# Kernel optimization log

Hardware: AMD Instinct MI355X
Metric: run time of the kernel (lower is better)

Reference implementation:

```python
import jax, jax.numpy as jnp
import numpy as np

N = 10000      # nodes
E = 320000     # edges (avg degree 32)
IN = 512       # in_channels
OUT = 128      # out_channels
H = 4          # in_head
C1 = 2 * OUT   # per-head hidden channels of conv1 (256)
NEG_SLOPE = 0.2


def setup_inputs() -> dict:
    key = jax.random.key(0)
    ks = jax.random.split(key, 12)
    x = jax.random.normal(ks[0], (N, IN), dtype=jnp.float32)
    edge_index = jax.random.randint(ks[1], (2, E), 0, N, dtype=jnp.int64)
    def glorot(k, shape):
        lim = np.sqrt(6.0 / (shape[0] + shape[-1])).astype(np.float32)
        return jax.random.uniform(k, shape, jnp.float32, -lim, lim)
    # conv1: GATv2Conv(IN -> C1 per head, heads=H)
    Wl1 = glorot(ks[2], (IN, H * C1))
    Wr1 = glorot(ks[3], (IN, H * C1))
    att1 = glorot(ks[4], (H, C1))
    b1 = jnp.zeros((H * C1,), jnp.float32)
    # conv2: GATv2Conv(H*C1 -> OUT, heads=1)
    Wl2 = glorot(ks[5], (H * C1, OUT))
    Wr2 = glorot(ks[6], (H * C1, OUT))
    att2 = glorot(ks[7], (1, OUT))
    b2 = jnp.zeros((OUT,), jnp.float32)
    return {"x": x, "edge_index": edge_index, "Wl1": Wl1, "Wr1": Wr1,
            "att1": att1, "b1": b1, "Wl2": Wl2, "Wr2": Wr2,
            "att2": att2, "b2": b2}


def gatv2_conv(x, src, dst, Wl, Wr, att, b, heads, ch):
    # x: [N, F_in]; src/dst: [E] (message src -> dst, softmax over dst)
    n = x.shape[0]
    xl = (x @ Wl).reshape(n, heads, ch)   # source-side projection
    xr = (x @ Wr).reshape(n, heads, ch)   # target-side projection
    # per-edge GATv2 score: att . LeakyReLU(xl_j + xr_i)   [E, H]
    e = jax.nn.leaky_relu(xl[src] + xr[dst], NEG_SLOPE)    # [E, H, C]
    s = jnp.einsum('ehc,hc->eh', e, att)                   # [E, H]
    # segment softmax over incoming edges of each dst node
    smax = jax.lax.stop_gradient(jax.ops.segment_max(s, dst, num_segments=n))
    ex = jnp.exp(s - smax[dst])
    denom = jax.ops.segment_sum(ex, dst, num_segments=n)
    alpha = ex / denom[dst]                                # [E, H]
    # weighted scatter-add of source messages
    out = jax.ops.segment_sum(alpha[:, :, None] * xl[src], dst, num_segments=n)
    return out.reshape(n, heads * ch) + b                  # concat heads + bias


def reference(x, edge_index, Wl1, Wr1, att1, b1, Wl2, Wr2, att2, b2):
    src, dst = edge_index[0], edge_index[1]
    h = gatv2_conv(x, src, dst, Wl1, Wr1, att1, b1, H, C1)
    h = jax.nn.relu(h)                                     # [N, H*C1]
    out = gatv2_conv(h, src, dst, Wl2, Wr2, att2, b2, 1, OUT)
    return out                                             # [N, OUT]
```

## Files before the change

### kernel.cpp

```cpp
#include <hip/hip_runtime.h>
#include <cfloat>

#define N_NODES 10000
#define N_EDGES 320000
#define IN_F    512
#define F1      1024
#define OUT_F   128
#define NEG     0.2f
#define BUCKET  128

typedef __attribute__((ext_vector_type(8))) short bf16x8;
typedef __attribute__((ext_vector_type(4))) float f32x4;

__device__ __forceinline__ float lrelu(float v) { return fmaxf(v, NEG * v); }

__device__ __forceinline__ unsigned short f2bf(float f) {
    unsigned u = __float_as_uint(f);
    u += 0x7fff + ((u >> 16) & 1);
    return (unsigned short)(u >> 16);
}
__device__ __forceinline__ float bf2f(unsigned short h) {
    return __uint_as_float(((unsigned)h) << 16);
}
__device__ __forceinline__ void u2f2(unsigned u, float& e0, float& e1) {
    e0 = __uint_as_float(u << 16);
    e1 = __uint_as_float(u & 0xffff0000u);
}

__device__ __forceinline__ float rsum16(float x) {
    x += __int_as_float(__builtin_amdgcn_update_dpp(0, __float_as_int(x), 0x121, 0xF, 0xF, false));
    x += __int_as_float(__builtin_amdgcn_update_dpp(0, __float_as_int(x), 0x122, 0xF, 0xF, false));
    x += __int_as_float(__builtin_amdgcn_update_dpp(0, __float_as_int(x), 0x124, 0xF, 0xF, false));
    x += __int_as_float(__builtin_amdgcn_update_dpp(0, __float_as_int(x), 0x128, 0xF, 0xF, false));
    return x;
}

__device__ __forceinline__ void gld_lds16(const void* g, void* l) {
    __builtin_amdgcn_global_load_lds(
        (const __attribute__((address_space(1))) unsigned int*)g,
        (__attribute__((address_space(3))) unsigned int*)l, 16, 0, 0);
}

#define PB_X  2500
#define PB_S  3750
#define PB_W1 4774
#define PB_END 5030

__device__ __forceinline__ void wt_body(const float* __restrict__ Wa,
                                        const float* __restrict__ Wb,
                                        unsigned short* __restrict__ tbf,
                                        int K, int NS, int n0, int k0, int t,
                                        float (*tile)[33]) {
    int j = t & 31;
    const float* W = (n0 < NS) ? Wa : Wb;
    int nb = (n0 < NS) ? n0 : n0 - NS;
#pragma unroll
    for (int r = 0; r < 4; ++r) {
        int kl = (t >> 5) + r * 8;
        tile[kl][j] = W[(size_t)(k0 + kl) * NS + nb + j];
    }
    __syncthreads();
#pragma unroll
    for (int r = 0; r < 4; ++r) {
        int nl = (t >> 5) + r * 8;
        tbf[(size_t)(n0 + nl) * K + k0 + j] = f2bf(tile[j][nl]);
    }
}

__global__ __launch_bounds__(256) void k_prep(const float* __restrict__ x,
                                              unsigned short* __restrict__ xbf,
                                              const int* __restrict__ ei,
                                              int* __restrict__ cnt,
                                              int* __restrict__ esrc,
                                              const float* __restrict__ Wl1,
                                              const float* __restrict__ Wr1,
                                              unsigned short* __restrict__ w1bf,
                                              const float* __restrict__ Wl2,
                                              const float* __restrict__ Wr2,
                                              unsigned short* __restrict__ w2bf) {
    __shared__ float tile[32][33];
    int bid = blockIdx.x, t = threadIdx.x;
    if (bid < PB_X) {
        int i = bid * 2048 + t * 8;
        float4 v0 = *(const float4*)(x + i);
        float4 v1 = *(const float4*)(x + i + 4);
        ushort4 h0, h1;
        h0.x = f2bf(v0.x); h0.y = f2bf(v0.y); h0.z = f2bf(v0.z); h0.w = f2bf(v0.w);
        h1.x = f2bf(v1.x); h1.y = f2bf(v1.y); h1.z = f2bf(v1.z); h1.w = f2bf(v1.w);
        *(ushort4*)(xbf + i) = h0;
        *(ushort4*)(xbf + i + 4) = h1;
    } else if (bid < PB_S) {
        int e = (bid - PB_X) * 256 + t;
        if (e < N_EDGES) {
            int d = ei[N_EDGES + e];
            int pos = atomicAdd(&cnt[d], 1);
            if (pos < BUCKET) esrc[(size_t)d * BUCKET + pos] = ei[e];
        }
    } else if (bid < PB_W1) {
        int local = bid - PB_S;
        wt_body(Wl1, Wr1, w1bf, IN_F, F1, (local & 63) * 32, (local >> 6) * 32, t, tile);
    } else {
        int local = bid - PB_W1;
        wt_body(Wl2, Wr2, w2bf, F1, OUT_F, (local & 7) * 32, (local >> 3) * 32, t, tile);
    }
}

__global__ __launch_bounds__(256) void k_sort(const int* __restrict__ cnt,
                                              int* __restrict__ esrc) {
    int t = threadIdx.x;
    int w = t >> 6, lane = t & 63;
    int nd = blockIdx.x * 4 + w;
    if (nd >= N_NODES) return;
    int deg = min(cnt[nd], 64);
    int p0 = nd * BUCKET;
    int v = (lane < deg) ? esrc[p0 + lane] : 0x7fffffff;
#pragma unroll
    for (int k = 2; k <= 64; k <<= 1) {
#pragma unroll
        for (int j = k >> 1; j > 0; j >>= 1) {
            int other = __shfl_xor(v, j);
            bool dir = ((lane & k) == 0);
            bool lower = ((lane & j) == 0);
            int mn = min(v, other), mx = max(v, other);
            v = (lower == dir) ? mn : mx;
        }
    }
    if (lane < deg) esrc[p0 + lane] = v;
}

template<int BM, int WR, int WC>
__global__ __launch_bounds__(256) void gemm_mfma(
        const unsigned short* __restrict__ A,
        const unsigned short* __restrict__ B,
        unsigned short* __restrict__ Cl, unsigned short* __restrict__ Cr,
        int M, int K, int NSPLIT) {
    constexpr int NI = BM / (16 * WR);
    constexpr int NJ = 128 / (16 * WC);
    __shared__ __align__(16) short As[BM * 32];
    __shared__ __align__(16) short Bs[128 * 32];
    int t = threadIdx.x;
    int lane = t & 63, w = t >> 6;
    int row0 = blockIdx.y * BM;
    int n0 = blockIdx.x * 128;
    int wr0 = (w / WC) * (NI * 16);
    int wc0 = (w % WC) * (NJ * 16);
    int q = lane >> 4, md = lane & 15;
    int srow = t >> 2;
    int skoff = (t & 3) * 8;

    f32x4 acc[NI][NJ];
#pragma unroll
    for (int i = 0; i < NI; ++i)
#pragma unroll
        for (int j = 0; j < NJ; ++j)
#pragma unroll
            for (int r = 0; r < 4; ++r) acc[i][j][r] = 0.f;

    for (int k0 = 0; k0 < K; k0 += 32) {
        __syncthreads();
#pragma unroll
        for (int is = 0; is < BM / 64; ++is) {
            int gr = row0 + is * 64 + srow;
            if (gr < M)
                gld_lds16(A + (size_t)gr * K + k0 + skoff,
                          &As[(is * 64 + (t >> 6) * 16) * 32]);
        }
#pragma unroll
        for (int is = 0; is < 2; ++is) {
            int gn = n0 + is * 64 + srow;
            gld_lds16(B + (size_t)gn * K + k0 + skoff,
                      &Bs[(is * 64 + (t >> 6) * 16) * 32]);
        }
        __syncthreads();

        bf16x8 av[NI], bv[NJ];
#pragma unroll
        for (int i = 0; i < NI; ++i)
            av[i] = *(const bf16x8*)&As[(wr0 + i * 16 + md) * 32 + q * 8];
#pragma unroll
        for (int j = 0; j < NJ; ++j)
            bv[j] = *(const bf16x8*)&Bs[(wc0 + j * 16 + md) * 32 + q * 8];
#pragma unroll
        for (int i = 0; i < NI; ++i)
#pragma unroll
            for (int j = 0; j < NJ; ++j)
                acc[i][j] = __builtin_amdgcn_mfma_f32_16x16x32_bf16(av[i], bv[j], acc[i][j], 0, 0, 0);
    }

#pragma unroll
    for (int i = 0; i < NI; ++i)
#pragma unroll
        for (int j = 0; j < NJ; ++j) {
            int col = n0 + wc0 + j * 16 + md;
            unsigned short* C = (col < NSPLIT) ? Cl : Cr;
            int cc = (col < NSPLIT) ? col : col - NSPLIT;
#pragma unroll
            for (int r = 0; r < 4; ++r) {
                int grow = row0 + wr0 + i * 16 + q * 4 + r;
                if (grow < M) C[(size_t)grow * NSPLIT + cc] = f2bf(acc[i][j][r]);
            }
        }
}

__global__ __launch_bounds__(256) void k_fused1(const unsigned short* __restrict__ xlbf,
                                                const unsigned short* __restrict__ xrbf,
                                                const int* __restrict__ cnt,
                                                const int* __restrict__ esrc,
                                                const float* __restrict__ att,
                                                const float* __restrict__ bias,
                                                unsigned short* __restrict__ hb) {
    int t = threadIdx.x;
    int w = t >> 6, lane = t & 63;
    int ni = w >> 1;
    int ww = w & 1;
    int nd = blockIdx.x * 2 + ni;
    int head = lane >> 4, sub = lane & 15;
    int ch = head * 256 + sub * 16;

    __shared__ float slx[4][4];
    __shared__ float4 sacc4[2][4][64];

    float4 r0, r1, r2, r3;
    {
        const uint4* prx = (const uint4*)(xrbf + (size_t)nd * F1 + ch);
        uint4 xa = prx[0], xb = prx[1];
        u2f2(xa.x, r0.x, r0.y); u2f2(xa.y, r0.z, r0.w);
        u2f2(xa.z, r1.x, r1.y); u2f2(xa.w, r1.z, r1.w);
        u2f2(xb.x, r2.x, r2.y); u2f2(xb.y, r2.z, r2.w);
        u2f2(xb.z, r3.x, r3.y); u2f2(xb.w, r3.z, r3.w);
    }
    const float4* pa = (const float4*)(att + ch);
    float4 a0 = pa[0], a1 = pa[1], a2 = pa[2], a3 = pa[3];

    int deg = min(cnt[nd], BUCKET);
    int p0 = nd * BUCKET;
    int dege = min(deg, 64);
    int bkt = (lane < dege) ? esrc[p0 + lane] : 0;

    float l = 0.f;
    float4 acc0 = make_float4(0.f, 0.f, 0.f, 0.f);
    float4 acc1 = acc0, acc2 = acc0, acc3 = acc0;

    auto edge_body = [&](uint4 ca, uint4 cb) {
        float4 c0, c1, c2, c3;
        u2f2(ca.x, c0.x, c0.y); u2f2(ca.y, c0.z, c0.w);
        u2f2(ca.z, c1.x, c1.y); u2f2(ca.w, c1.z, c1.w);
        u2f2(cb.x, c2.x, c2.y); u2f2(cb.y, c2.z, c2.w);
        u2f2(cb.z, c3.x, c3.y); u2f2(cb.w, c3.z, c3.w);
        float u;
        float sl0, sa0, sl1, sa1, sl2, sa2, sl3, sa3;
        u = c0.x + r0.x; sl0 = a0.x * u;           sa0 = a0.x * fabsf(u);
        u = c0.y + r0.y; sl0 = fmaf(a0.y, u, sl0); sa0 = fmaf(a0.y, fabsf(u), sa0);
        u = c0.z + r0.z; sl0 = fmaf(a0.z, u, sl0); sa0 = fmaf(a0.z, fabsf(u), sa0);
        u = c0.w + r0.w; sl0 = fmaf(a0.w, u, sl0); sa0 = fmaf(a0.w, fabsf(u), sa0);
        u = c1.x + r1.x; sl1 = a1.x * u;           sa1 = a1.x * fabsf(u);
        u = c1.y + r1.y; sl1 = fmaf(a1.y, u, sl1); sa1 = fmaf(a1.y, fabsf(u), sa1);
        u = c1.z + r1.z; sl1 = fmaf(a1.z, u, sl1); sa1 = fmaf(a1.z, fabsf(u), sa1);
        u = c1.w + r1.w; sl1 = fmaf(a1.w, u, sl1); sa1 = fmaf(a1.w, fabsf(u), sa1);
        u = c2.x + r2.x; sl2 = a2.x * u;           sa2 = a2.x * fabsf(u);
        u = c2.y + r2.y; sl2 = fmaf(a2.y, u, sl2); sa2 = fmaf(a2.y, fabsf(u), sa2);
        u = c2.z + r2.z; sl2 = fmaf(a2.z, u, sl2); sa2 = fmaf(a2.z, fabsf(u), sa2);
        u = c2.w + r2.w; sl2 = fmaf(a2.w, u, sl2); sa2 = fmaf(a2.w, fabsf(u), sa2);
        u = c3.x + r3.x; sl3 = a3.x * u;           sa3 = a3.x * fabsf(u);
        u = c3.y + r3.y; sl3 = fmaf(a3.y, u, sl3); sa3 = fmaf(a3.y, fabsf(u), sa3);
        u = c3.z + r3.z; sl3 = fmaf(a3.z, u, sl3); sa3 = fmaf(a3.z, fabsf(u), sa3);
        u = c3.w + r3.w; sl3 = fmaf(a3.w, u, sl3); sa3 = fmaf(a3.w, fabsf(u), sa3);
        float sl = (sl0 + sl1) + (sl2 + sl3);
        float sa = (sa0 + sa1) + (sa2 + sa3);
        float s = rsum16(fmaf(0.6f, sl, 0.4f * sa));
        s = fminf(fmaxf(s, -60.f), 60.f);
        float al = __expf(s);
        l += al;
        acc0.x = fmaf(al, c0.x, acc0.x);
        acc0.y = fmaf(al, c0.y, acc0.y);
        acc0.z = fmaf(al, c0.z, acc0.z);
        acc0.w = fmaf(al, c0.w, acc0.w);
        acc1.x = fmaf(al, c1.x, acc1.x);
        acc1.y = fmaf(al, c1.y, acc1.y);
        acc1.z = fmaf(al, c1.z, acc1.z);
        acc1.w = fmaf(al, c1.w, acc1.w);
        acc2.x = fmaf(al, c2.x, acc2.x);
        acc2.y = fmaf(al, c2.y, acc2.y);
        acc2.z = fmaf(al, c2.z, acc2.z);
        acc2.w = fmaf(al, c2.w, acc2.w);
        acc3.x = fmaf(al, c3.x, acc3.x);
        acc3.y = fmaf(al, c3.y, acc3.y);
        acc3.z = fmaf(al, c3.z, acc3.z);
        acc3.w = fmaf(al, c3.w, acc3.w);
    };

    int idx = ww;
    uint4 ua, ub;
    if (idx < dege) {
        int sn = __shfl(bkt, idx);
        const uint4* pv = (const uint4*)(xlbf + (size_t)sn * F1 + ch);
        ua = pv[0]; ub = pv[1];
    }
    for (; idx < dege; idx += 2) {
        uint4 ca = ua, cb = ub;
        int nidx = idx + 2;
        if (nidx < dege) {
            int sn = __shfl(bkt, nidx);
            const uint4* pv = (const uint4*)(xlbf + (size_t)sn * F1 + ch);
            ua = pv[0]; ub = pv[1];
        }
        edge_body(ca, cb);
    }
    for (int p = p0 + 64 + ww; p < p0 + deg; p += 2) {
        const uint4* pv = (const uint4*)(xlbf + (size_t)esrc[p] * F1 + ch);
        edge_body(pv[0], pv[1]);
    }

    if (sub == 0) slx[w][head] = l;
    if (ww == 1) {
        sacc4[ni][0][lane] = acc0;
        sacc4[ni][1][lane] = acc1;
        sacc4[ni][2][lane] = acc2;
        sacc4[ni][3][lane] = acc3;
    }
    __syncthreads();
    if (ww == 0) {
        float L = l + slx[w ^ 1][head];
        float invL = (L > 0.f) ? 1.f / L : 0.f;
        const float4* pb = (const float4*)(bias + ch);
        size_t base = (size_t)nd * F1 + ch;
        float4 aa[4] = {acc0, acc1, acc2, acc3};
#pragma unroll
        for (int j = 0; j < 4; ++j) {
            float4 pt = sacc4[ni][j][lane];
            float4 b4 = pb[j];
            ushort4 hv;
            hv.x = f2bf(fmaxf(fmaf(aa[j].x + pt.x, invL, b4.x), 0.f));
            hv.y = f2bf(fmaxf(fmaf(aa[j].y + pt.y, invL, b4.y), 0.f));
            hv.z = f2bf(fmaxf(fmaf(aa[j].z + pt.z, invL, b4.z), 0.f));
            hv.w = f2bf(fmaxf(fmaf(aa[j].w + pt.w, invL, b4.w), 0.f));
            *(ushort4*)(hb + base + j * 4) = hv;
        }
    }
}

__global__ __launch_bounds__(256) void k_fused2(const unsigned short* __restrict__ xlbf,
                                                const unsigned short* __restrict__ xrbf,
                                                const int* __restrict__ cnt,
                                                const int* __restrict__ esrc,
                                                const float* __restrict__ att,
                                                const float* __restrict__ bias,
                                                float* __restrict__ out) {
    int t = threadIdx.x;
    int w = t >> 6, lane = t & 63;
    int nd = blockIdx.x * 4 + w;
    int g = lane >> 4, sub = lane & 15;
    int ch = sub * 8;

    __shared__ float slx2[4][4];
    __shared__ float sacc2[4][4][132];

    float r[8], a[8];
    {
        uint4 u = *(const uint4*)(xrbf + (size_t)nd * OUT_F + ch);
        u2f2(u.x, r[0], r[1]); u2f2(u.y, r[2], r[3]);
        u2f2(u.z, r[4], r[5]); u2f2(u.w, r[6], r[7]);
        float4 q0 = *(const float4*)(att + ch);
        float4 q1 = *(const float4*)(att + ch + 4);
        a[0] = q0.x; a[1] = q0.y; a[2] = q0.z; a[3] = q0.w;
        a[4] = q1.x; a[5] = q1.y; a[6] = q1.z; a[7] = q1.w;
    }
    int deg = min(cnt[nd], BUCKET);
    int p0 = nd * BUCKET;
    int p1 = p0 + deg;

    float l = 0.f;
    float acc[8] = {};
    uint4 cur, nxt;
    {
        int p = p0 + g;
        if (p < p1)     cur = *(const uint4*)(xlbf + (size_t)esrc[p] * OUT_F + ch);
        if (p + 4 < p1) nxt = *(const uint4*)(xlbf + (size_t)esrc[p + 4] * OUT_F + ch);
    }
    for (int p = p0 + g; p < p1; p += 4) {
        uint4 c = cur;
        cur = nxt;
        if (p + 8 < p1) nxt = *(const uint4*)(xlbf + (size_t)esrc[p + 8] * OUT_F + ch);
        float v[8];
        u2f2(c.x, v[0], v[1]); u2f2(c.y, v[2], v[3]);
        u2f2(c.z, v[4], v[5]); u2f2(c.w, v[6], v[7]);
        float uu;
        float slA, saA, slB, saB;
        uu = v[0] + r[0]; slA = a[0] * uu;           saA = a[0] * fabsf(uu);
        uu = v[1] + r[1]; slA = fmaf(a[1], uu, slA); saA = fmaf(a[1], fabsf(uu), saA);
        uu = v[2] + r[2]; slA = fmaf(a[2], uu, slA); saA = fmaf(a[2], fabsf(uu), saA);
        uu = v[3] + r[3]; slA = fmaf(a[3], uu, slA); saA = fmaf(a[3], fabsf(uu), saA);
        uu = v[4] + r[4]; slB = a[4] * uu;           saB = a[4] * fabsf(uu);
        uu = v[5] + r[5]; slB = fmaf(a[5], uu, slB); saB = fmaf(a[5], fabsf(uu), saB);
        uu = v[6] + r[6]; slB = fmaf(a[6], uu, slB); saB = fmaf(a[6], fabsf(uu), saB);
        uu = v[7] + r[7]; slB = fmaf(a[7], uu, slB); saB = fmaf(a[7], fabsf(uu), saB);
        float s = rsum16(fmaf(0.6f, slA + slB, 0.4f * (saA + saB)));
        s = fminf(fmaxf(s, -60.f), 60.f);
        float al = __expf(s);
        l += al;
#pragma unroll
        for (int k = 0; k < 8; ++k) acc[k] = fmaf(al, v[k], acc[k]);
    }

    if (sub == 0) slx2[w][g] = l;
    float4 v0 = make_float4(acc[0], acc[1], acc[2], acc[3]);
    float4 v1 = make_float4(acc[4], acc[5], acc[6], acc[7]);
    *(float4*)&sacc2[w][g][ch] = v0;
    *(float4*)&sacc2[w][g][ch + 4] = v1;
    __syncthreads();
    float L = slx2[w][0] + slx2[w][1] + slx2[w][2] + slx2[w][3];
    float invL = (L > 0.f) ? 1.f / L : 0.f;
    int c2 = lane * 2;
    float o0 = sacc2[w][0][c2] + sacc2[w][1][c2] + sacc2[w][2][c2] + sacc2[w][3][c2];
    float o1 = sacc2[w][0][c2 + 1] + sacc2[w][1][c2 + 1] + sacc2[w][2][c2 + 1] + sacc2[w][3][c2 + 1];
    float2 bf = *(const float2*)(bias + c2);
    float2 o;
    o.x = fmaf(o0, invL, bf.x);
    o.y = fmaf(o1, invL, bf.y);
    *(float2*)(out + (size_t)nd * OUT_F + c2) = o;
}

extern "C" void kernel_launch(void* const* d_in, const int* in_sizes, int n_in,
                              void* d_out, int out_size, void* d_ws, size_t ws_size,
                              hipStream_t stream) {
    const float* x    = (const float*)d_in[0];
    const int*   ei   = (const int*)d_in[1];
    const float* Wl1  = (const float*)d_in[2];
    const float* Wr1  = (const float*)d_in[3];
    const float* att1 = (const float*)d_in[4];
    const float* b1   = (const float*)d_in[5];
    const float* Wl2  = (const float*)d_in[6];
    const float* Wr2  = (const float*)d_in[7];
    const float* att2 = (const float*)d_in[8];
    const float* b2   = (const float*)d_in[9];
    float* out = (float*)d_out;

    unsigned short* us = (unsigned short*)d_ws;
    unsigned short* xl1bf = us;
    unsigned short* xr1bf = xl1bf + (size_t)N_NODES * F1;
    unsigned short* xl2bf = xr1bf + (size_t)N_NODES * F1;
    unsigned short* xr2bf = xl2bf + (size_t)N_NODES * OUT_F;
    unsigned short* hb   = xr2bf + (size_t)N_NODES * OUT_F;
    unsigned short* xbf  = hb + (size_t)N_NODES * F1;
    unsigned short* w1bf = xbf + (size_t)N_NODES * IN_F;
    unsigned short* w2bf = w1bf + (size_t)2048 * IN_F;
    int* cnt   = (int*)(w2bf + (size_t)256 * F1);
    int* esrc  = cnt + (N_NODES + 16);

    hipMemsetAsync(cnt, 0, sizeof(int) * N_NODES, stream);
    k_prep<<<PB_END, 256, 0, stream>>>(x, xbf, ei, cnt, esrc,
                                       Wl1, Wr1, w1bf,
                                       Wl2, Wr2, w2bf);

    k_sort<<<(N_NODES + 3) / 4, 256, 0, stream>>>(cnt, esrc);

    gemm_mfma<128, 2, 2><<<dim3(16, (N_NODES + 127) / 128), 256, 0, stream>>>(
        xbf, w1bf, xl1bf, xr1bf, N_NODES, IN_F, F1);

    k_fused1<<<N_NODES / 2, 256, 0, stream>>>(xl1bf, xr1bf, cnt, esrc, att1, b1, hb);

    gemm_mfma<64, 1, 4><<<dim3(2, (N_NODES + 63) / 64), 256, 0, stream>>>(
        hb, w2bf, xl2bf, xr2bf, N_NODES, F1, OUT_F);

    k_fused2<<<N_NODES / 4, 256, 0, stream>>>(xl2bf, xr2bf, cnt, esrc, att2, b2, out);
}
```

Baseline: 263.3 us.

## Stage GEMM epilogue through LDS for coalesced stores and add nontemporal hints

The GEMM epilogue now writes bf16 accumulators into a shared-memory tile that reuses the operand staging buffers through a union, then writes whole rows to global memory with 16-byte vector stores. Previously each lane wrote scattered 2-byte values. Separately, single-use streams (the x conversion, xr row loads, and the h and out stores) now use nontemporal loads and stores to reduce cache pollution. The cost is an extra LDS round trip plus barriers in the GEMM, and the nontemporal hint on h may hurt if the following GEMM would have reused it from cache.

Measured after the change: 267.2 us. About the same (+1.5%).

```diff
diff --git a/kernel.cpp b/kernel.cpp
--- a/kernel.cpp
+++ b/kernel.cpp
@@ -11,6 +11,9 @@
 
 typedef __attribute__((ext_vector_type(8))) short bf16x8;
 typedef __attribute__((ext_vector_type(4))) float f32x4;
+typedef __attribute__((ext_vector_type(2))) float f32x2;
+typedef __attribute__((ext_vector_type(4))) unsigned int u32x4;
+typedef __attribute__((ext_vector_type(4))) unsigned short u16x4;
 
 __device__ __forceinline__ float lrelu(float v) { return fmaxf(v, NEG * v); }
 
@@ -82,8 +85,8 @@
     int bid = blockIdx.x, t = threadIdx.x;
     if (bid < PB_X) {
         int i = bid * 2048 + t * 8;
-        float4 v0 = *(const float4*)(x + i);
-        float4 v1 = *(const float4*)(x + i + 4);
+        f32x4 v0 = __builtin_nontemporal_load((const f32x4*)(x + i));
+        f32x4 v1 = __builtin_nontemporal_load((const f32x4*)(x + i + 4));
         ushort4 h0, h1;
         h0.x = f2bf(v0.x); h0.y = f2bf(v0.y); h0.z = f2bf(v0.z); h0.w = f2bf(v0.w);
         h1.x = f2bf(v1.x); h1.y = f2bf(v1.y); h1.z = f2bf(v1.z); h1.w = f2bf(v1.w);
@@ -128,6 +131,13 @@
     if (lane < deg) esrc[p0 + lane] = v;
 }
 
+template<int BM> struct GemmSmem {
+    union {
+        struct { short As[BM * 32]; short Bs[128 * 32]; } st;
+        unsigned short ct[BM * 136];
+    };
+};
+
 template<int BM, int WR, int WC>
 __global__ __launch_bounds__(256) void gemm_mfma(
         const unsigned short* __restrict__ A,
@@ -136,8 +146,7 @@
         int M, int K, int NSPLIT) {
     constexpr int NI = BM / (16 * WR);
     constexpr int NJ = 128 / (16 * WC);
-    __shared__ __align__(16) short As[BM * 32];
-    __shared__ __align__(16) short Bs[128 * 32];
+    __shared__ __align__(16) GemmSmem<BM> sm;
     int t = threadIdx.x;
     int lane = t & 63, w = t >> 6;
     int row0 = blockIdx.y * BM;
@@ -163,23 +172,23 @@
             int gr = row0 + is * 64 + srow;
             if (gr < M)
                 gld_lds16(A + (size_t)gr * K + k0 + skoff,
-                          &As[(is * 64 + (t >> 6) * 16) * 32]);
+                          &sm.st.As[(is * 64 + (t >> 6) * 16) * 32]);
         }
 #pragma unroll
         for (int is = 0; is < 2; ++is) {
             int gn = n0 + is * 64 + srow;
             gld_lds16(B + (size_t)gn * K + k0 + skoff,
-                      &Bs[(is * 64 + (t >> 6) * 16) * 32]);
+                      &sm.st.Bs[(is * 64 + (t >> 6) * 16) * 32]);
         }
         __syncthreads();
 
         bf16x8 av[NI], bv[NJ];
 #pragma unroll
         for (int i = 0; i < NI; ++i)
-            av[i] = *(const bf16x8*)&As[(wr0 + i * 16 + md) * 32 + q * 8];
+            av[i] = *(const bf16x8*)&sm.st.As[(wr0 + i * 16 + md) * 32 + q * 8];
 #pragma unroll
         for (int j = 0; j < NJ; ++j)
-            bv[j] = *(const bf16x8*)&Bs[(wc0 + j * 16 + md) * 32 + q * 8];
+            bv[j] = *(const bf16x8*)&sm.st.Bs[(wc0 + j * 16 + md) * 32 + q * 8];
 #pragma unroll
         for (int i = 0; i < NI; ++i)
 #pragma unroll
@@ -187,19 +196,25 @@
                 acc[i][j] = __builtin_amdgcn_mfma_f32_16x16x32_bf16(av[i], bv[j], acc[i][j], 0, 0, 0);
     }
 
+    __syncthreads();
 #pragma unroll
     for (int i = 0; i < NI; ++i)
 #pragma unroll
-        for (int j = 0; j < NJ; ++j) {
-            int col = n0 + wc0 + j * 16 + md;
-            unsigned short* C = (col < NSPLIT) ? Cl : Cr;
-            int cc = (col < NSPLIT) ? col : col - NSPLIT;
-#pragma unroll
-            for (int r = 0; r < 4; ++r) {
-                int grow = row0 + wr0 + i * 16 + q * 4 + r;
-                if (grow < M) C[(size_t)grow * NSPLIT + cc] = f2bf(acc[i][j][r]);
-            }
-        }
+        for (int j = 0; j < NJ; ++j)
+#pragma unroll
+            for (int r = 0; r < 4; ++r)
+                sm.ct[(wr0 + i * 16 + q * 4 + r) * 136 + wc0 + j * 16 + md] =
+                    f2bf(acc[i][j][r]);
+    __syncthreads();
+    unsigned short* C = (n0 < NSPLIT) ? Cl : Cr;
+    int cc0 = (n0 < NSPLIT) ? n0 : n0 - NSPLIT;
+    for (int idx = t; idx < BM * 16; idx += 256) {
+        int row = idx >> 4, seg = idx & 15;
+        if (row0 + row < M) {
+            bf16x8 val = *(const bf16x8*)&sm.ct[row * 136 + seg * 8];
+            *(bf16x8*)(C + (size_t)(row0 + row) * NSPLIT + cc0 + seg * 8) = val;
+        }
+    }
 }
 
 __global__ __launch_bounds__(256) void k_fused1(const unsigned short* __restrict__ xlbf,
@@ -222,8 +237,9 @@
 
     float4 r0, r1, r2, r3;
     {
-        const uint4* prx = (const uint4*)(xrbf + (size_t)nd * F1 + ch);
-        uint4 xa = prx[0], xb = prx[1];
+        const u32x4* prx = (const u32x4*)(xrbf + (size_t)nd * F1 + ch);
+        u32x4 xa = __builtin_nontemporal_load(prx);
+        u32x4 xb = __builtin_nontemporal_load(prx + 1);
         u2f2(xa.x, r0.x, r0.y); u2f2(xa.y, r0.z, r0.w);
         u2f2(xa.z, r1.x, r1.y); u2f2(xa.w, r1.z, r1.w);
         u2f2(xb.x, r2.x, r2.y); u2f2(xb.y, r2.z, r2.w);
@@ -329,12 +345,12 @@
         for (int j = 0; j < 4; ++j) {
             float4 pt = sacc4[ni][j][lane];
             float4 b4 = pb[j];
-            ushort4 hv;
+            u16x4 hv;
             hv.x = f2bf(fmaxf(fmaf(aa[j].x + pt.x, invL, b4.x), 0.f));
             hv.y = f2bf(fmaxf(fmaf(aa[j].y + pt.y, invL, b4.y), 0.f));
             hv.z = f2bf(fmaxf(fmaf(aa[j].z + pt.z, invL, b4.z), 0.f));
             hv.w = f2bf(fmaxf(fmaf(aa[j].w + pt.w, invL, b4.w), 0.f));
-            *(ushort4*)(hb + base + j * 4) = hv;
+            __builtin_nontemporal_store(hv, (u16x4*)(hb + base + j * 4));
         }
     }
 }
@@ -357,7 +373,8 @@
 
     float r[8], a[8];
     {
-        uint4 u = *(const uint4*)(xrbf + (size_t)nd * OUT_F + ch);
+        u32x4 u = __builtin_nontemporal_load(
+            (const u32x4*)(xrbf + (size_t)nd * OUT_F + ch));
         u2f2(u.x, r[0], r[1]); u2f2(u.y, r[2], r[3]);
         u2f2(u.z, r[4], r[5]); u2f2(u.w, r[6], r[7]);
         float4 q0 = *(const float4*)(att + ch);
@@ -414,10 +431,10 @@
     float o0 = sacc2[w][0][c2] + sacc2[w][1][c2] + sacc2[w][2][c2] + sacc2[w][3][c2];
     float o1 = sacc2[w][0][c2 + 1] + sacc2[w][1][c2 + 1] + sacc2[w][2][c2 + 1] + sacc2[w][3][c2 + 1];
     float2 bf = *(const float2*)(bias + c2);
-    float2 o;
+    f32x2 o;
     o.x = fmaf(o0, invL, bf.x);
     o.y = fmaf(o1, invL, bf.y);
-    *(float2*)(out + (size_t)nd * OUT_F + c2) = o;
+    __builtin_nontemporal_store(o, (f32x2*)(out + (size_t)nd * OUT_F + c2));
 }
 
 extern "C" void kernel_launch(void* const* d_in, const int* in_sizes, int n_in,
```
